# Performance work log

Hardware: AMD Instinct MI355X
Metric: run time of the kernel (lower is better)

## Reference

```python
import jax, jax.numpy as jnp
import numpy as np

NOT_EPSILON = 1.0
W_SCALE = 0.05  # scaled randn init for numerical stability of swishmax logits

H, T, A, C = 8, 1024, 64, 256  # heads, key/query size, attention size, compress size


def swishmax(x, axis):
    m = jnp.max(x, axis=axis, keepdims=True)
    xe = x * jnp.exp(x - m)
    return xe / (jnp.sum(jnp.abs(xe), axis=axis, keepdims=True) + NOT_EPSILON)


def setup_inputs() -> dict:
    key = jax.random.key(0)
    ks = jax.random.split(key, 7)
    B, Q, K = 2, 2048, 2048
    return {
        "query_tokens": jax.random.normal(ks[0], (B, Q, T), dtype=jnp.float32),
        "key_tokens": jax.random.normal(ks[1], (B, K, T), dtype=jnp.float32),
        "key_down": jax.random.normal(ks[2], (H, T, A), dtype=jnp.float32) * W_SCALE,
        "query_down": jax.random.normal(ks[3], (H, T, A), dtype=jnp.float32) * W_SCALE,
        "query_down_bias": jax.random.normal(ks[4], (H, 1, A), dtype=jnp.float32) * W_SCALE,
        "value_down": jax.random.normal(ks[5], (H, T, C), dtype=jnp.float32) * W_SCALE,
        "value_up": jax.random.normal(ks[6], (H, C, T), dtype=jnp.float32) * W_SCALE,
    }


def reference(query_tokens, key_tokens, key_down, query_down, query_down_bias, value_down, value_up):
    # key/query projections: [B,K,T] x [H,T,A] -> [B,H,K,A]
    k = jnp.einsum('bkt,hta->bhka', key_tokens, key_down)
    q = jnp.einsum('bqt,hta->bhqa', query_tokens, query_down) + query_down_bias[None]  # [B,H,Q,A]
    # attention logits: key @ query^T -> [B,H,K,Q]
    logits = jnp.einsum('bhka,bhqa->bhkq', k, q)
    attn = swishmax(logits, axis=-2)  # normalized over keys (dim=-2)
    # sum_k key_tokens[b,k,:] * attn[b,h,k,q]  ==  [B,H,Q,T] (matmul form of the outer-product sum)
    vs = jnp.einsum('bhkq,bkt->bhqt', attn, key_tokens)
    # compress path: value_down then value_up
    vs = jnp.einsum('bhqc,hct->bhqt', jnp.einsum('bhqt,htc->bhqc', vs, value_down), value_up)
    return vs.sum(axis=1)  # sum over heads -> [B,Q,T]
```

## Files before the change

### kernel.cpp

```cpp
#include <hip/hip_runtime.h>
#include <hip/hip_fp16.h>
#include <math.h>


typedef _Float16 f16;
typedef _Float16 f16x4 __attribute__((ext_vector_type(4)));
typedef _Float16 f16x8 __attribute__((ext_vector_type(8)));
typedef short s16x4 __attribute__((ext_vector_type(4)));
typedef short bf16x8 __attribute__((ext_vector_type(8)));
typedef float f32x4 __attribute__((ext_vector_type(4)));

#define MFMA_F16(a, b, c) __builtin_amdgcn_mfma_f32_16x16x32_f16(a, b, c, 0, 0, 0)
#define MFMA_BF16(a, b, c) __builtin_amdgcn_mfma_f32_16x16x32_bf16(a, b, c, 0, 0, 0)

__device__ __forceinline__ void g2lds16(const void* g, void* l) {
  __builtin_amdgcn_global_load_lds((__attribute__((address_space(1))) void*)g,
                                   (__attribute__((address_space(3))) void*)l, 16, 0, 0);
}

__device__ __forceinline__ short f32_bf16(float x) {
  union { float f; unsigned u; } v; v.f = x;
  unsigned r = v.u + 0x7FFFu + ((v.u >> 16) & 1u);
  return (short)(r >> 16);
}
__device__ __forceinline__ float bf16_f32(short h) {
  union { unsigned u; float f; } v; v.u = ((unsigned)(unsigned short)h) << 16;
  return v.f;
}

__global__ __launch_bounds__(256) void ew_split(const float* __restrict__ in,
                                                short* __restrict__ bhi,
                                                short* __restrict__ blo,
                                                f16* __restrict__ fo, int n4) {
  int i = blockIdx.x * 256 + threadIdx.x;
  int stride = gridDim.x * 256;
  for (; i < n4; i += stride) {
    f32x4 v = ((const f32x4*)in)[i];
    s16x4 h, l;
    f16x4 f;
#pragma unroll
    for (int j = 0; j < 4; j++) {
      short hj = f32_bf16(v[j]);
      h[j] = hj;
      l[j] = f32_bf16(v[j] - bf16_f32(hj));
      f[j] = (f16)v[j];
    }
    ((s16x4*)bhi)[i] = h;
    ((s16x4*)blo)[i] = l;
    if (fo) ((f16x4*)fo)[i] = f;
  }
}

__global__ __launch_bounds__(256) void transpose_split(const float* __restrict__ in,
                                                       short* __restrict__ bhi,
                                                       short* __restrict__ blo,
                                                       f16* __restrict__ fo,
                                                       int R, int C) {
  __shared__ float t[64][65];
  int cb = blockIdx.x * 64, rb = blockIdx.y * 64;
  size_t batch = (size_t)blockIdx.z * R * C;
  int tid = threadIdx.x;
#pragma unroll
  for (int i = 0; i < 4; i++) {
    int r = (tid >> 4) + i * 16, c4 = (tid & 15) * 4;
    f32x4 v = *(const f32x4*)(in + batch + (size_t)(rb + r) * C + cb + c4);
    t[r][c4] = v[0]; t[r][c4 + 1] = v[1]; t[r][c4 + 2] = v[2]; t[r][c4 + 3] = v[3];
  }
  __syncthreads();
#pragma unroll
  for (int i = 0; i < 4; i++) {
    int c = (tid >> 4) + i * 16, r4 = (tid & 15) * 4;
    float v0 = t[r4][c], v1 = t[r4 + 1][c], v2 = t[r4 + 2][c], v3 = t[r4 + 3][c];
    size_t o = batch + (size_t)(cb + c) * R + rb + r4;
    if (bhi) {
      s16x4 h = {f32_bf16(v0), f32_bf16(v1), f32_bf16(v2), f32_bf16(v3)};
      *(s16x4*)(bhi + o) = h;
      s16x4 l = {f32_bf16(v0 - bf16_f32(h[0])), f32_bf16(v1 - bf16_f32(h[1])),
                 f32_bf16(v2 - bf16_f32(h[2])), f32_bf16(v3 - bf16_f32(h[3]))};
      *(s16x4*)(blo + o) = l;
    }
    if (fo) {
      f16x4 fv = {(f16)v0, (f16)v1, (f16)v2, (f16)v3};
      *(f16x4*)(fo + o) = fv;
    }
  }
}

__global__ __launch_bounds__(256, 2) void proj_gemm(
    const short* __restrict__ qtok_hi, const short* __restrict__ qtok_lo,
    const short* __restrict__ ktok_hi, const short* __restrict__ ktok_lo,
    const short* __restrict__ wqT_hi, const short* __restrict__ wqT_lo,
    const short* __restrict__ wkT_hi, const short* __restrict__ wkT_lo,
    const float* __restrict__ bias, short* __restrict__ q_split,
    short* __restrict__ k_split) {
  const bool isQ = (blockIdx.z == 0);
  const short* Ahi = isQ ? qtok_hi : ktok_hi;
  const short* Alo = isQ ? qtok_lo : ktok_lo;
  const short* Bhi = isQ ? wqT_hi : wkT_hi;
  const short* Blo = isQ ? wqT_lo : wkT_lo;
  short* outp = isQ ? q_split : k_split;

  __shared__ __attribute__((aligned(16))) short sm[4][128 * 32];

  int tid = threadIdx.x, w = tid >> 6, lane = tid & 63, g = lane >> 4, li = lane & 15;
  int mb = blockIdx.y * 128, nb = blockIdx.x * 128;
  int wm = (w >> 1) * 64, wn = (w & 1) * 64;

  f32x4 acc[4][4] = {};

  for (int kb = 0; kb < 1024; kb += 32) {
    __syncthreads();
#pragma unroll
    for (int i = 0; i < 2; i++) {
      int off = (w * 2 + i) * 1024 + lane * 16;
      int row = off >> 6;
      int ss = ((off >> 4) & 3) ^ ((row >> 1) & 3);
      size_t asrc = (size_t)(mb + row) * 1024 + kb + ss * 8;
      size_t bsrc = (size_t)(nb + row) * 1024 + kb + ss * 8;
      int dst = (w * 2 + i) * 512;
      g2lds16(Ahi + asrc, &sm[0][dst]);
      g2lds16(Alo + asrc, &sm[1][dst]);
      g2lds16(Bhi + bsrc, &sm[2][dst]);
      g2lds16(Blo + bsrc, &sm[3][dst]);
    }
    __syncthreads();
    bf16x8 af[4][2], bf[4][2];
#pragma unroll
    for (int f = 0; f < 4; f++) {
      int ra = wm + f * 16 + li;
      int sa = g ^ ((ra >> 1) & 3);
      af[f][0] = *(const bf16x8*)&sm[0][ra * 32 + sa * 8];
      af[f][1] = *(const bf16x8*)&sm[1][ra * 32 + sa * 8];
      int rb = wn + f * 16 + li;
      int sb = g ^ ((rb >> 1) & 3);
      bf[f][0] = *(const bf16x8*)&sm[2][rb * 32 + sb * 8];
      bf[f][1] = *(const bf16x8*)&sm[3][rb * 32 + sb * 8];
    }
#pragma unroll
    for (int mf = 0; mf < 4; mf++)
#pragma unroll
      for (int nf = 0; nf < 4; nf++) {
        acc[mf][nf] = MFMA_BF16(af[mf][0], bf[nf][0], acc[mf][nf]);
        acc[mf][nf] = MFMA_BF16(af[mf][0], bf[nf][1], acc[mf][nf]);
        acc[mf][nf] = MFMA_BF16(af[mf][1], bf[nf][0], acc[mf][nf]);
      }
  }
#pragma unroll
  for (int mf = 0; mf < 4; mf++)
#pragma unroll
    for (int nf = 0; nf < 4; nf++)
#pragma unroll
      for (int r = 0; r < 4; r++) {
        int m = mb + wm + mf * 16 + 4 * g + r;
        int n = nb + wn + nf * 16 + li;
        float v = acc[mf][nf][r];
        if (isQ) v += bias[n];
        short hi = f32_bf16(v);
        short lo = f32_bf16(v - bf16_f32(hi));
        size_t base = ((size_t)((m >> 11) * 8 + (n >> 6)) * 2048 + (m & 2047)) * 128;
        outp[base + (n & 63)] = hi;
        outp[base + 64 + (n & 63)] = lo;
      }
}

__global__ __launch_bounds__(256, 2) void kv_gemm(const f16* __restrict__ A,
                                                  const f16* __restrict__ Bm,
                                                  f16* __restrict__ kvT) {
  __shared__ __attribute__((aligned(16))) f16 sm[2][128 * 32];
  int tid = threadIdx.x, w = tid >> 6, lane = tid & 63, g = lane >> 4, li = lane & 15;
  int mb = blockIdx.y * 128, nb = blockIdx.x * 128;
  int wm = (w >> 1) * 64, wn = (w & 1) * 64;
  f32x4 acc[4][4] = {};
  for (int kb = 0; kb < 1024; kb += 32) {
    __syncthreads();
#pragma unroll
    for (int i = 0; i < 2; i++) {
      int off = (w * 2 + i) * 1024 + lane * 16;
      int row = off >> 6;
      int ss = ((off >> 4) & 3) ^ ((row >> 1) & 3);
      int dst = (w * 2 + i) * 512;
      g2lds16(A + (size_t)(mb + row) * 1024 + kb + ss * 8, &sm[0][dst]);
      g2lds16(Bm + (size_t)(nb + row) * 1024 + kb + ss * 8, &sm[1][dst]);
    }
    __syncthreads();
    f16x8 af[4], bf[4];
#pragma unroll
    for (int f = 0; f < 4; f++) {
      int ra = wm + f * 16 + li;
      int sa = g ^ ((ra >> 1) & 3);
      af[f] = *(const f16x8*)&sm[0][ra * 32 + sa * 8];
      int rb = wn + f * 16 + li;
      int sb = g ^ ((rb >> 1) & 3);
      bf[f] = *(const f16x8*)&sm[1][rb * 32 + sb * 8];
    }
#pragma unroll
    for (int mf = 0; mf < 4; mf++)
#pragma unroll
      for (int nf = 0; nf < 4; nf++)
        acc[mf][nf] = MFMA_F16(af[mf], bf[nf], acc[mf][nf]);
  }
#pragma unroll
  for (int mf = 0; mf < 4; mf++)
#pragma unroll
    for (int nf = 0; nf < 4; nf++) {
      int m = mb + wm + mf * 16 + 4 * g;
      int n = nb + wn + nf * 16 + li;
      f16x4 v = {(f16)acc[mf][nf][0], (f16)acc[mf][nf][1], (f16)acc[mf][nf][2],
                 (f16)acc[mf][nf][3]};
      size_t o = ((size_t)((m >> 11) * 8 + (n >> 8)) * 256 + (n & 255)) * 2048 + (m & 2047);
      *(f16x4*)(kvT + o) = v;
    }
}

__global__ __launch_bounds__(256, 2) void flash_attn(const short* __restrict__ q_split,
                                                     const short* __restrict__ k_split,
                                                     const f16* __restrict__ kvT,
                                                     f16* __restrict__ vs_c) {
  __shared__ __attribute__((aligned(16))) short k_lds[32 * 128];
  __shared__ __attribute__((aligned(16))) f16 kv_lds[256 * 32];
  __shared__ __attribute__((aligned(16))) f16 p_lds[4][640];

  const int bid = blockIdx.x;
  const int bh = ((bid & 7) << 1) + ((bid >> 3) & 1);
  const int qb = bid >> 4;
  const int tid = threadIdx.x;
  const int w = tid >> 6, lane = tid & 63, g = lane >> 4, li = lane & 15;

  const short* qrow = q_split + ((size_t)bh * 2048 + qb * 64 + w * 16 + li) * 128;
  bf16x8 qf[2][2];
#pragma unroll
  for (int ach = 0; ach < 2; ach++)
#pragma unroll
    for (int hl = 0; hl < 2; hl++)
      qf[ach][hl] = *(const bf16x8*)(qrow + hl * 64 + ach * 32 + g * 8);

  const short* kbase = k_split + (size_t)bh * 2048 * 128;
  const f16* kvbase = kvT + (size_t)bh * 256 * 2048;

  float m_cur = -INFINITY, m_true = -INFINITY, l_run = 0.f;
  f32x4 acc[16] = {};

  for (int kt = 0; kt < 64; kt++) {
    __syncthreads();
#pragma unroll
    for (int i = 0; i < 2; i++) {
      int off = (w * 2 + i) * 1024 + lane * 16;
      int row = off >> 8;
      int ss = ((off >> 4) & 15) ^ (row & 7);
      g2lds16(kbase + (size_t)(kt * 32 + row) * 128 + ss * 8,
              (char*)k_lds + (w * 2 + i) * 1024);
    }
#pragma unroll
    for (int i = 0; i < 4; i++) {
      int off = (w * 4 + i) * 1024 + lane * 16;
      int c = off >> 6;
      int ss = ((off >> 4) & 3) ^ ((c >> 1) & 3);
      g2lds16(kvbase + (size_t)c * 2048 + kt * 32 + ss * 8,
              (char*)kv_lds + (w * 4 + i) * 1024);
    }
    __syncthreads();

    f32x4 s[2] = {};
#pragma unroll
    for (int kc = 0; kc < 2; kc++) {
      const int r = kc * 16 + li;
#pragma unroll
      for (int ach = 0; ach < 2; ach++) {
        int sh = (ach * 4 + g) ^ (r & 7);
        int sl = (8 + ach * 4 + g) ^ (r & 7);
        bf16x8 khi = *(const bf16x8*)((const char*)k_lds + r * 256 + sh * 16);
        bf16x8 klo = *(const bf16x8*)((const char*)k_lds + r * 256 + sl * 16);
        s[kc] = MFMA_BF16(khi, qf[ach][0], s[kc]);
        s[kc] = MFMA_BF16(khi, qf[ach][1], s[kc]);
        s[kc] = MFMA_BF16(klo, qf[ach][0], s[kc]);
      }
    }

    float tmax = fmaxf(fmaxf(fmaxf(s[0][0], s[0][1]), fmaxf(s[0][2], s[0][3])),
                       fmaxf(fmaxf(s[1][0], s[1][1]), fmaxf(s[1][2], s[1][3])));
    tmax = fmaxf(tmax, __shfl_xor(tmax, 16));
    tmax = fmaxf(tmax, __shfl_xor(tmax, 32));
    m_true = fmaxf(m_true, tmax);
    if (__any(tmax > m_cur + 4.0f)) {
      float mn = fmaxf(m_cur, tmax);
      float sc = __expf(m_cur - mn);
      l_run *= sc;
#pragma unroll
      for (int i = 0; i < 16; i++) acc[i] *= sc;
      m_cur = mn;
    }
    float ls = 0.f;
    float pv[8];
#pragma unroll
    for (int kc = 0; kc < 2; kc++)
#pragma unroll
      for (int r2 = 0; r2 < 4; r2++) {
        float sv = s[kc][r2];
        float e = sv * __expf(sv - m_cur);
        pv[kc * 4 + r2] = e;
        ls += fabsf(e);
      }
    ls += __shfl_xor(ls, 16);
    ls += __shfl_xor(ls, 32);
    l_run += ls;

#pragma unroll
    for (int kc = 0; kc < 2; kc++) {
      f16x4 p4 = {(f16)pv[kc * 4], (f16)pv[kc * 4 + 1], (f16)pv[kc * 4 + 2],
                  (f16)pv[kc * 4 + 3]};
      *(f16x4*)&p_lds[w][li * 40 + kc * 16 + 4 * g] = p4;
    }
    f16x8 pf = *(const f16x8*)&p_lds[w][li * 40 + 8 * g];

#pragma unroll
    for (int ct = 0; ct < 16; ct++) {
      int c = ct * 16 + li;
      int ss = g ^ ((c >> 1) & 3);
      f16x8 vf = *(const f16x8*)((const char*)kv_lds + c * 64 + ss * 16);
      acc[ct] = MFMA_F16(vf, pf, acc[ct]);
    }
  }

  float sfix = __expf(m_cur - m_true);
  float invd = sfix / (l_run * sfix + 1.0f);
  f16* orow = vs_c + ((size_t)(bh >> 3) * 2048 + qb * 64 + w * 16 + li) * 2048 + (bh & 7) * 256;
#pragma unroll
  for (int ct = 0; ct < 16; ct++) {
    f16x4 v = {(f16)(acc[ct][0] * invd), (f16)(acc[ct][1] * invd),
               (f16)(acc[ct][2] * invd), (f16)(acc[ct][3] * invd)};
    *(f16x4*)(orow + ct * 16 + 4 * g) = v;
  }
}

__global__ __launch_bounds__(256, 2) void final_gemm(const f16* __restrict__ A,
                                                     const f16* __restrict__ Bm,
                                                     float* __restrict__ outp) {
  __shared__ __attribute__((aligned(16))) f16 sm[2][128 * 32];
  int tid = threadIdx.x, w = tid >> 6, lane = tid & 63, g = lane >> 4, li = lane & 15;
  int mb = blockIdx.y * 128, nb = blockIdx.x * 128;
  int wm = (w >> 1) * 64, wn = (w & 1) * 64;
  f32x4 acc[4][4] = {};
  for (int kb = 0; kb < 2048; kb += 32) {
    __syncthreads();
#pragma unroll
    for (int i = 0; i < 2; i++) {
      int off = (w * 2 + i) * 1024 + lane * 16;
      int row = off >> 6;
      int ss = ((off >> 4) & 3) ^ ((row >> 1) & 3);
      int dst = (w * 2 + i) * 512;
      g2lds16(A + (size_t)(mb + row) * 2048 + kb + ss * 8, &sm[0][dst]);
      g2lds16(Bm + (size_t)(nb + row) * 2048 + kb + ss * 8, &sm[1][dst]);
    }
    __syncthreads();
    f16x8 af[4], bf[4];
#pragma unroll
    for (int f = 0; f < 4; f++) {
      int ra = wm + f * 16 + li;
      int sa = g ^ ((ra >> 1) & 3);
      af[f] = *(const f16x8*)&sm[0][ra * 32 + sa * 8];
      int rb = wn + f * 16 + li;
      int sb = g ^ ((rb >> 1) & 3);
      bf[f] = *(const f16x8*)&sm[1][rb * 32 + sb * 8];
    }
#pragma unroll
    for (int mf = 0; mf < 4; mf++)
#pragma unroll
      for (int nf = 0; nf < 4; nf++)
        acc[mf][nf] = MFMA_F16(af[mf], bf[nf], acc[mf][nf]);
  }
#pragma unroll
  for (int mf = 0; mf < 4; mf++)
#pragma unroll
    for (int nf = 0; nf < 4; nf++)
#pragma unroll
      for (int r = 0; r < 4; r++) {
        int m = mb + wm + mf * 16 + 4 * g + r;
        int n = nb + wn + nf * 16 + li;
        outp[(size_t)m * 1024 + n] = acc[mf][nf][r];
      }
}

extern "C" void kernel_launch(void* const* d_in, const int* in_sizes, int n_in,
                              void* d_out, int out_size, void* d_ws, size_t ws_size,
                              hipStream_t stream) {
  (void)in_sizes; (void)n_in; (void)out_size; (void)ws_size;
  const float* qtok = (const float*)d_in[0];
  const float* ktok = (const float*)d_in[1];
  const float* kdw = (const float*)d_in[2];
  const float* qdw = (const float*)d_in[3];
  const float* qdb = (const float*)d_in[4];
  const float* vdw = (const float*)d_in[5];
  const float* vup = (const float*)d_in[6];

  char* ws = (char*)d_ws;
  size_t off = 0;
  auto take = [&](size_t n) { void* p = ws + off; off += (n + 255) & ~(size_t)255; return p; };

  short* qtok_hi = (short*)take(8u << 20);
  short* qtok_lo = (short*)take(8u << 20);
  short* ktok_hi = (short*)take(8u << 20);
  short* ktok_lo = (short*)take(8u << 20);
  f16* ktok_f = (f16*)take(8u << 20);
  short* wqT_hi = (short*)take(1u << 20);
  short* wqT_lo = (short*)take(1u << 20);
  short* wkT_hi = (short*)take(1u << 20);
  short* wkT_lo = (short*)take(1u << 20);
  f16* vdT = (f16*)take(4u << 20);
  f16* vuT = (f16*)take(4u << 20);
  short* q_split = (short*)take(8u << 20);
  short* k_split = (short*)take(8u << 20);
  f16* kvT = (f16*)(void*)ktok_hi;
  f16* vs_c = (f16*)(void*)qtok_hi;

  ew_split<<<2048, 256, 0, stream>>>(qtok, qtok_hi, qtok_lo, (f16*)nullptr, 1048576);
  ew_split<<<2048, 256, 0, stream>>>(ktok, ktok_hi, ktok_lo, ktok_f, 1048576);
  transpose_split<<<dim3(1, 16, 8), 256, 0, stream>>>(qdw, wqT_hi, wqT_lo, nullptr, 1024, 64);
  transpose_split<<<dim3(1, 16, 8), 256, 0, stream>>>(kdw, wkT_hi, wkT_lo, nullptr, 1024, 64);
  transpose_split<<<dim3(4, 16, 8), 256, 0, stream>>>(vdw, nullptr, nullptr, vdT, 1024, 256);
  transpose_split<<<dim3(16, 32, 1), 256, 0, stream>>>(vup, nullptr, nullptr, vuT, 2048, 1024);

  proj_gemm<<<dim3(4, 32, 2), 256, 0, stream>>>(qtok_hi, qtok_lo, ktok_hi, ktok_lo,
                                                wqT_hi, wqT_lo, wkT_hi, wkT_lo, qdb,
                                                q_split, k_split);
  kv_gemm<<<dim3(16, 32), 256, 0, stream>>>(ktok_f, vdT, kvT);
  flash_attn<<<512, 256, 0, stream>>>(q_split, k_split, kvT, vs_c);
  final_gemm<<<dim3(8, 32), 256, 0, stream>>>(vs_c, vuT, (float*)d_out);
}
```

Measured before the change: 243.4 us.

## Double-buffer LDS tiles in all GEMM and attention kernels, prioritize MFMA sections

Each of the four kernels now has two LDS buffers. The next tile's global-to-LDS load is issued before the current tile is computed, so each iteration needs one barrier instead of two. Memory latency can then overlap with MFMA work. The flash attention kernel also raises wave priority (s_setprio) around its MFMA blocks. The cost is double the LDS per block, which could limit occupancy. The g2lds loads use async direct-to-LDS, and correctness relies on the barrier before the next buffer is read waiting for those loads to complete.

```diff
diff --git a/kernel.cpp b/kernel.cpp
--- a/kernel.cpp
+++ b/kernel.cpp
@@ -100,7 +100,7 @@
   const short* Blo = isQ ? wqT_lo : wkT_lo;
   short* outp = isQ ? q_split : k_split;
 
-  __shared__ __attribute__((aligned(16))) short sm[4][128 * 32];
+  __shared__ __attribute__((aligned(16))) short sm[2][4][128 * 32];
 
   int tid = threadIdx.x, w = tid >> 6, lane = tid & 63, g = lane >> 4, li = lane & 15;
   int mb = blockIdx.y * 128, nb = blockIdx.x * 128;
@@ -108,8 +108,7 @@
 
   f32x4 acc[4][4] = {};
 
-  for (int kb = 0; kb < 1024; kb += 32) {
-    __syncthreads();
+  auto STAGE = [&](int kb, int buf) {
 #pragma unroll
     for (int i = 0; i < 2; i++) {
       int off = (w * 2 + i) * 1024 + lane * 16;
@@ -118,23 +117,29 @@
       size_t asrc = (size_t)(mb + row) * 1024 + kb + ss * 8;
       size_t bsrc = (size_t)(nb + row) * 1024 + kb + ss * 8;
       int dst = (w * 2 + i) * 512;
-      g2lds16(Ahi + asrc, &sm[0][dst]);
-      g2lds16(Alo + asrc, &sm[1][dst]);
-      g2lds16(Bhi + bsrc, &sm[2][dst]);
-      g2lds16(Blo + bsrc, &sm[3][dst]);
-    }
-    __syncthreads();
+      g2lds16(Ahi + asrc, &sm[buf][0][dst]);
+      g2lds16(Alo + asrc, &sm[buf][1][dst]);
+      g2lds16(Bhi + bsrc, &sm[buf][2][dst]);
+      g2lds16(Blo + bsrc, &sm[buf][3][dst]);
+    }
+  };
+
+  STAGE(0, 0);
+  __syncthreads();
+  for (int kb = 0; kb < 1024; kb += 32) {
+    int cur = (kb >> 5) & 1;
+    if (kb + 32 < 1024) STAGE(kb + 32, cur ^ 1);
     bf16x8 af[4][2], bf[4][2];
 #pragma unroll
     for (int f = 0; f < 4; f++) {
       int ra = wm + f * 16 + li;
       int sa = g ^ ((ra >> 1) & 3);
-      af[f][0] = *(const bf16x8*)&sm[0][ra * 32 + sa * 8];
-      af[f][1] = *(const bf16x8*)&sm[1][ra * 32 + sa * 8];
+      af[f][0] = *(const bf16x8*)&sm[cur][0][ra * 32 + sa * 8];
+      af[f][1] = *(const bf16x8*)&sm[cur][1][ra * 32 + sa * 8];
       int rb = wn + f * 16 + li;
       int sb = g ^ ((rb >> 1) & 3);
-      bf[f][0] = *(const bf16x8*)&sm[2][rb * 32 + sb * 8];
-      bf[f][1] = *(const bf16x8*)&sm[3][rb * 32 + sb * 8];
+      bf[f][0] = *(const bf16x8*)&sm[cur][2][rb * 32 + sb * 8];
+      bf[f][1] = *(const bf16x8*)&sm[cur][3][rb * 32 + sb * 8];
     }
 #pragma unroll
     for (int mf = 0; mf < 4; mf++)
@@ -144,6 +149,7 @@
         acc[mf][nf] = MFMA_BF16(af[mf][0], bf[nf][1], acc[mf][nf]);
         acc[mf][nf] = MFMA_BF16(af[mf][1], bf[nf][0], acc[mf][nf]);
       }
+    __syncthreads();
   }
 #pragma unroll
   for (int mf = 0; mf < 4; mf++)
@@ -166,38 +172,45 @@
 __global__ __launch_bounds__(256, 2) void kv_gemm(const f16* __restrict__ A,
                                                   const f16* __restrict__ Bm,
                                                   f16* __restrict__ kvT) {
-  __shared__ __attribute__((aligned(16))) f16 sm[2][128 * 32];
+  __shared__ __attribute__((aligned(16))) f16 sm[2][2][128 * 32];
   int tid = threadIdx.x, w = tid >> 6, lane = tid & 63, g = lane >> 4, li = lane & 15;
   int mb = blockIdx.y * 128, nb = blockIdx.x * 128;
   int wm = (w >> 1) * 64, wn = (w & 1) * 64;
   f32x4 acc[4][4] = {};
-  for (int kb = 0; kb < 1024; kb += 32) {
-    __syncthreads();
+
+  auto STAGE = [&](int kb, int buf) {
 #pragma unroll
     for (int i = 0; i < 2; i++) {
       int off = (w * 2 + i) * 1024 + lane * 16;
       int row = off >> 6;
       int ss = ((off >> 4) & 3) ^ ((row >> 1) & 3);
       int dst = (w * 2 + i) * 512;
-      g2lds16(A + (size_t)(mb + row) * 1024 + kb + ss * 8, &sm[0][dst]);
-      g2lds16(Bm + (size_t)(nb + row) * 1024 + kb + ss * 8, &sm[1][dst]);
-    }
-    __syncthreads();
+      g2lds16(A + (size_t)(mb + row) * 1024 + kb + ss * 8, &sm[buf][0][dst]);
+      g2lds16(Bm + (size_t)(nb + row) * 1024 + kb + ss * 8, &sm[buf][1][dst]);
+    }
+  };
+
+  STAGE(0, 0);
+  __syncthreads();
+  for (int kb = 0; kb < 1024; kb += 32) {
+    int cur = (kb >> 5) & 1;
+    if (kb + 32 < 1024) STAGE(kb + 32, cur ^ 1);
     f16x8 af[4], bf[4];
 #pragma unroll
     for (int f = 0; f < 4; f++) {
       int ra = wm + f * 16 + li;
       int sa = g ^ ((ra >> 1) & 3);
-      af[f] = *(const f16x8*)&sm[0][ra * 32 + sa * 8];
+      af[f] = *(const f16x8*)&sm[cur][0][ra * 32 + sa * 8];
       int rb = wn + f * 16 + li;
       int sb = g ^ ((rb >> 1) & 3);
-      bf[f] = *(const f16x8*)&sm[1][rb * 32 + sb * 8];
+      bf[f] = *(const f16x8*)&sm[cur][1][rb * 32 + sb * 8];
     }
 #pragma unroll
     for (int mf = 0; mf < 4; mf++)
 #pragma unroll
       for (int nf = 0; nf < 4; nf++)
         acc[mf][nf] = MFMA_F16(af[mf], bf[nf], acc[mf][nf]);
+    __syncthreads();
   }
 #pragma unroll
   for (int mf = 0; mf < 4; mf++)
@@ -216,8 +229,8 @@
                                                      const short* __restrict__ k_split,
                                                      const f16* __restrict__ kvT,
                                                      f16* __restrict__ vs_c) {
-  __shared__ __attribute__((aligned(16))) short k_lds[32 * 128];
-  __shared__ __attribute__((aligned(16))) f16 kv_lds[256 * 32];
+  __shared__ __attribute__((aligned(16))) short k_lds[2][32 * 128];
+  __shared__ __attribute__((aligned(16))) f16 kv_lds[2][256 * 32];
   __shared__ __attribute__((aligned(16))) f16 p_lds[4][640];
 
   const int bid = blockIdx.x;
@@ -240,15 +253,14 @@
   float m_cur = -INFINITY, m_true = -INFINITY, l_run = 0.f;
   f32x4 acc[16] = {};
 
-  for (int kt = 0; kt < 64; kt++) {
-    __syncthreads();
+  auto STAGE = [&](int kt, int buf) {
 #pragma unroll
     for (int i = 0; i < 2; i++) {
       int off = (w * 2 + i) * 1024 + lane * 16;
       int row = off >> 8;
       int ss = ((off >> 4) & 15) ^ (row & 7);
       g2lds16(kbase + (size_t)(kt * 32 + row) * 128 + ss * 8,
-              (char*)k_lds + (w * 2 + i) * 1024);
+              (char*)k_lds[buf] + (w * 2 + i) * 1024);
     }
 #pragma unroll
     for (int i = 0; i < 4; i++) {
@@ -256,11 +268,19 @@
       int c = off >> 6;
       int ss = ((off >> 4) & 3) ^ ((c >> 1) & 3);
       g2lds16(kvbase + (size_t)c * 2048 + kt * 32 + ss * 8,
-              (char*)kv_lds + (w * 4 + i) * 1024);
-    }
-    __syncthreads();
+              (char*)kv_lds[buf] + (w * 4 + i) * 1024);
+    }
+  };
+
+  STAGE(0, 0);
+  __syncthreads();
+
+  for (int kt = 0; kt < 64; kt++) {
+    const int cur = kt & 1;
+    if (kt < 63) STAGE(kt + 1, cur ^ 1);
 
     f32x4 s[2] = {};
+    __builtin_amdgcn_s_setprio(1);
 #pragma unroll
     for (int kc = 0; kc < 2; kc++) {
       const int r = kc * 16 + li;
@@ -268,13 +288,14 @@
       for (int ach = 0; ach < 2; ach++) {
         int sh = (ach * 4 + g) ^ (r & 7);
         int sl = (8 + ach * 4 + g) ^ (r & 7);
-        bf16x8 khi = *(const bf16x8*)((const char*)k_lds + r * 256 + sh * 16);
-        bf16x8 klo = *(const bf16x8*)((const char*)k_lds + r * 256 + sl * 16);
+        bf16x8 khi = *(const bf16x8*)((const char*)k_lds[cur] + r * 256 + sh * 16);
+        bf16x8 klo = *(const bf16x8*)((const char*)k_lds[cur] + r * 256 + sl * 16);
         s[kc] = MFMA_BF16(khi, qf[ach][0], s[kc]);
         s[kc] = MFMA_BF16(khi, qf[ach][1], s[kc]);
         s[kc] = MFMA_BF16(klo, qf[ach][0], s[kc]);
       }
     }
+    __builtin_amdgcn_s_setprio(0);
 
     float tmax = fmaxf(fmaxf(fmaxf(s[0][0], s[0][1]), fmaxf(s[0][2], s[0][3])),
                        fmaxf(fmaxf(s[1][0], s[1][1]), fmaxf(s[1][2], s[1][3])));
@@ -312,13 +333,17 @@
     }
     f16x8 pf = *(const f16x8*)&p_lds[w][li * 40 + 8 * g];
 
+    __builtin_amdgcn_s_setprio(1);
 #pragma unroll
     for (int ct = 0; ct < 16; ct++) {
       int c = ct * 16 + li;
       int ss = g ^ ((c >> 1) & 3);
-      f16x8 vf = *(const f16x8*)((const char*)kv_lds + c * 64 + ss * 16);
+      f16x8 vf = *(const f16x8*)((const char*)kv_lds[cur] + c * 64 + ss * 16);
       acc[ct] = MFMA_F16(vf, pf, acc[ct]);
     }
+    __builtin_amdgcn_s_setprio(0);
+
+    __syncthreads();
   }
 
   float sfix = __expf(m_cur - m_true);
@@ -335,38 +360,45 @@
 __global__ __launch_bounds__(256, 2) void final_gemm(const f16* __restrict__ A,
                                                      const f16* __restrict__ Bm,
                                                      float* __restrict__ outp) {
-  __shared__ __attribute__((aligned(16))) f16 sm[2][128 * 32];
+  __shared__ __attribute__((aligned(16))) f16 sm[2][2][128 * 32];
   int tid = threadIdx.x, w = tid >> 6, lane = tid & 63, g = lane >> 4, li = lane & 15;
   int mb = blockIdx.y * 128, nb = blockIdx.x * 128;
   int wm = (w >> 1) * 64, wn = (w & 1) * 64;
   f32x4 acc[4][4] = {};
-  for (int kb = 0; kb < 2048; kb += 32) {
-    __syncthreads();
+
+  auto STAGE = [&](int kb, int buf) {
 #pragma unroll
     for (int i = 0; i < 2; i++) {
       int off = (w * 2 + i) * 1024 + lane * 16;
       int row = off >> 6;
       int ss = ((off >> 4) & 3) ^ ((row >> 1) & 3);
       int dst = (w * 2 + i) * 512;
-      g2lds16(A + (size_t)(mb + row) * 2048 + kb + ss * 8, &sm[0][dst]);
-      g2lds16(Bm + (size_t)(nb + row) * 2048 + kb + ss * 8, &sm[1][dst]);
-    }
-    __syncthreads();
+      g2lds16(A + (size_t)(mb + row) * 2048 + kb + ss * 8, &sm[buf][0][dst]);
+      g2lds16(Bm + (size_t)(nb + row) * 2048 + kb + ss * 8, &sm[buf][1][dst]);
+    }
+  };
+
+  STAGE(0, 0);
+  __syncthreads();
+  for (int kb = 0; kb < 2048; kb += 32) {
+    int cur = (kb >> 5) & 1;
+    if (kb + 32 < 2048) STAGE(kb + 32, cur ^ 1);
     f16x8 af[4], bf[4];
 #pragma unroll
     for (int f = 0; f < 4; f++) {
       int ra = wm + f * 16 + li;
       int sa = g ^ ((ra >> 1) & 3);
-      af[f] = *(const f16x8*)&sm[0][ra * 32 + sa * 8];
+      af[f] = *(const f16x8*)&sm[cur][0][ra * 32 + sa * 8];
       int rb = wn + f * 16 + li;
       int sb = g ^ ((rb >> 1) & 3);
-      bf[f] = *(const f16x8*)&sm[1][rb * 32 + sb * 8];
+      bf[f] = *(const f16x8*)&sm[cur][1][rb * 32 + sb * 8];
     }
 #pragma unroll
     for (int mf = 0; mf < 4; mf++)
 #pragma unroll
       for (int nf = 0; nf < 4; nf++)
         acc[mf][nf] = MFMA_F16(af[mf], bf[nf], acc[mf][nf]);
+    __syncthreads();
   }
 #pragma unroll
   for (int mf = 0; mf < 4; mf++)
```

Measured after the change: 228.3 us. 1.07x faster.
